# Kernel optimization log

Measured on AMD Instinct MI355X. Metric: run time of the kernel, lower is better.

## Reference

```python
import jax, jax.numpy as jnp
import numpy as np

EMBED = 192
EXPAND = 3
D1 = EMBED * EXPAND  # 576
RPE_IN = 32
LAYERS = 3
LAMBDA = 0.95


def _rpe_mlp(t, w0, b0, ws, bs, wo, bo):
    # t: (2n, 1) relative positions -> (2n, D1) Toeplitz coefficients
    h = t @ w0.T + b0
    for i in range(ws.shape[0]):
        h = jax.nn.relu(h) @ ws[i].T + bs[i]
    return jax.nn.relu(h) @ wo.T + bo


def _toeplitz(x, a):
    # Toeplitz matmul via length-2n circular convolution (FFT).
    # x: (B, n, d); a: (2n, d) coeffs ordered [t0, t1..t_{n-1}, pad, neg half]
    n = x.shape[1]
    m = 2 * n
    xf = jnp.fft.rfft(x, m, axis=1)
    af = jnp.fft.rfft(a, m, axis=0)
    return jnp.fft.irfft(xf * af[None], m, axis=1)[:, :n]


def _forward(x, p_w, p_b, q_w, q_b, v_w, v_b, o_w, o_b, slope,
             t1_w0, t1_b0, t1_ws, t1_bs, t1_wo, t1_bo,
             t2_w0, t2_b0, t2_ws, t2_bs, t2_wo, t2_bo):
    b, h, w, d = x.shape
    n = h  # square grid: h == w, rpe/decay built from n = x.shape[1]
    dt = x.dtype

    pos = jnp.arange(1, n, dtype=dt).reshape(-1, 1)          # (n-1, 1)
    zero = jnp.zeros((1, 1), dt)
    rpe_input = jnp.concatenate([zero, pos, zero, -pos], axis=0)  # (2n, 1)

    p = jax.nn.silu(x @ p_w.T + p_b)
    q = jax.nn.silu(x @ q_w.T + q_b)
    v = jax.nn.silu(x @ v_w.T + v_b)

    # decay mask: slope clamped to [0,1], blended with lambda, powered by |lag|
    sl = LAMBDA + (1.0 - LAMBDA) * jnp.clip(slope, 0.0, 1.0)  # (1, D1)
    idx = jnp.arange(1, n, dtype=dt).reshape(1, -1, 1)        # (1, n-1, 1)
    gamma = sl ** idx                                          # (1, n-1, D1)
    one = jnp.ones((1, 1, D1), dt)
    decay = jnp.concatenate([one, gamma, one, gamma[:, ::-1]], axis=1)[0]  # (2n, D1)

    a1 = _rpe_mlp(rpe_input, t1_w0, t1_b0, t1_ws, t1_bs, t1_wo, t1_bo) * decay
    a2 = _rpe_mlp(rpe_input, t2_w0, t2_b0, t2_ws, t2_bs, t2_wo, t2_bo) * decay

    qv = q * v                                                 # (b, h, w, D1)
    # axial mixing: tno1 along width, tno2 along height
    o1 = _toeplitz(qv.reshape(b * h, w, D1), a1).reshape(b, h, w, D1)
    o2 = _toeplitz(jnp.transpose(qv, (0, 2, 1, 3)).reshape(b * w, h, D1), a2)
    o2 = jnp.transpose(o2.reshape(b, w, h, D1), (0, 2, 1, 3))
    out = p * (o1 + o2)
    return out @ o_w.T + o_b


def setup_inputs() -> dict:
    key = jax.random.key(0)
    ks = jax.random.split(key, 8)

    def lin(k, out_d, in_d):
        k1, k2 = jax.random.split(k)
        s = 1.0 / np.sqrt(in_d)
        return (jax.random.uniform(k1, (out_d, in_d), jnp.float32, -s, s),
                jax.random.uniform(k2, (out_d,), jnp.float32, -s, s))

    x = jax.random.normal(ks[0], (8, 56, 56, EMBED), jnp.float32)
    p_w, p_b = lin(ks[1], D1, EMBED)
    q_w, q_b = lin(ks[2], D1, EMBED)
    v_w, v_b = lin(ks[3], D1, EMBED)
    o_w, o_b = lin(ks[4], EMBED, D1)
    # slope init: 1/arange(1, d1+1)^(1/(index+1)), index=0
    slope = (1.0 / jnp.arange(1, D1 + 1, dtype=jnp.float32)).reshape(1, -1)

    def tno_params(kb):
        kk = jax.random.split(kb, 2 + LAYERS)
        w0, b0 = lin(kk[0], RPE_IN, 1)
        ws, bs = [], []
        for i in range(LAYERS):
            wi, bi = lin(kk[1 + i], RPE_IN, RPE_IN)
            ws.append(wi); bs.append(bi)
        wo, bo = lin(kk[1 + LAYERS], D1, RPE_IN)
        return w0, b0, jnp.stack(ws), jnp.stack(bs), wo, bo

    t1 = tno_params(ks[5])
    t2 = tno_params(ks[6])
    return {"x": x, "p_w": p_w, "p_b": p_b, "q_w": q_w, "q_b": q_b,
            "v_w": v_w, "v_b": v_b, "o_w": o_w, "o_b": o_b, "slope": slope,
            "t1_w0": t1[0], "t1_b0": t1[1], "t1_ws": t1[2], "t1_bs": t1[3], "t1_wo": t1[4], "t1_bo": t1[5],
            "t2_w0": t2[0], "t2_b0": t2[1], "t2_ws": t2[2], "t2_bs": t2[3], "t2_wo": t2[4], "t2_bo": t2[5]}


def reference(x, p_w, p_b, q_w, q_b, v_w, v_b, o_w, o_b, slope,
              t1_w0, t1_b0, t1_ws, t1_bs, t1_wo, t1_bo,
              t2_w0, t2_b0, t2_ws, t2_bs, t2_wo, t2_bo):
    return _forward(x, p_w, p_b, q_w, q_b, v_w, v_b, o_w, o_b, slope,
                    t1_w0, t1_b0, t1_ws, t1_bs, t1_wo, t1_bo,
                    t2_w0, t2_b0, t2_ws, t2_bs, t2_wo, t2_bo)
```

## Files before the change

### kernel.cpp

```cpp
#include <hip/hip_runtime.h>
#include <hip/hip_bf16.h>
#include <math.h>

typedef unsigned short u16;
typedef short bf16x8 __attribute__((ext_vector_type(8)));
typedef float f32x4 __attribute__((ext_vector_type(4)));

#define NB 8
#define NN 56
#define M2 112
#define EMB 192
#define D1 576
#define TOK (NB*NN*NN)

__device__ __forceinline__ float bf2f(unsigned int u) {
    union { unsigned int i; float f; } v; v.i = u << 16; return v.f;
}
__device__ __forceinline__ u16 f2bf(float f) {
    union { float f; unsigned int i; } v; v.f = f;
    unsigned int x = v.i;
    return (u16)((x + 0x7fffu + ((x >> 16) & 1u)) >> 16);
}
__device__ __forceinline__ float silu(float x) {
    return x / (1.0f + __expf(-x));
}
__device__ __forceinline__ void async16(void* lds, const void* g) {
    __builtin_amdgcn_global_load_lds(
        (const __attribute__((address_space(1))) void*)g,
        (__attribute__((address_space(3))) void*)lds, 16, 0, 0);
}

#define XCH (TOK*EMB/4)
#define WCH (D1*EMB/4)
__global__ __launch_bounds__(256) void convert_kernel(
    const float* __restrict__ x,
    const float* __restrict__ pw, const float* __restrict__ qw,
    const float* __restrict__ vw, const float* __restrict__ ow,
    u16* __restrict__ xb, u16* __restrict__ wb, u16* __restrict__ owb)
{
    int tid = blockIdx.x * 256 + threadIdx.x;
    const float* src; u16* dst; int off;
    if (tid < XCH) { src = x; dst = xb; off = tid; }
    else {
        int r = tid - XCH;
        int seg = r / WCH; off = r % WCH;
        if (seg == 0)      { src = pw; dst = wb; }
        else if (seg == 1) { src = qw; dst = wb + D1*EMB; }
        else if (seg == 2) { src = vw; dst = wb + 2*D1*EMB; }
        else if (seg == 3) { src = ow; dst = owb; }
        else return;
    }
    float4 f = *(const float4*)(src + off * 4);
    ushort4 o;
    o.x = f2bf(f.x); o.y = f2bf(f.y); o.z = f2bf(f.z); o.w = f2bf(f.w);
    *(ushort4*)(dst + off * 4) = o;
}

__global__ __launch_bounds__(576) void rpe_kernel(
    const float* __restrict__ slope,
    const float* w0a, const float* b0a, const float* wsa, const float* bsa,
    const float* woa, const float* boa,
    const float* w0b, const float* b0b, const float* wsb, const float* bsb,
    const float* wob, const float* bob,
    float* __restrict__ A1, float* __restrict__ A2)
{
    int wq  = blockIdx.x / M2;
    int row = blockIdx.x % M2;
    const float* w0 = wq ? w0b : w0a;  const float* b0 = wq ? b0b : b0a;
    const float* ws = wq ? wsb : wsa;  const float* bs = wq ? bsb : bsa;
    const float* wo = wq ? wob : woa;  const float* bo = wq ? bob : boa;
    float* A = wq ? A2 : A1;

    float tval = (row == 0 || row == 56) ? 0.0f
               : (row < 56 ? (float)row : -(float)(row - 56));
    int kexp = (row == 0 || row == 56) ? 0 : (row < 56 ? row : 112 - row);

    __shared__ float h[32], g[32];
    int t = threadIdx.x;
    if (t < 32) h[t] = tval * w0[t] + b0[t];
    __syncthreads();
    for (int L = 0; L < 3; L++) {
        if (t < 32) g[t] = fmaxf(h[t], 0.0f);
        __syncthreads();
        float hn = 0.0f;
        if (t < 32) {
            hn = bs[L * 32 + t];
            for (int k = 0; k < 32; k++)
                hn = fmaf(g[k], ws[(L * 32 + t) * 32 + k], hn);
        }
        __syncthreads();
        if (t < 32) h[t] = hn;
        __syncthreads();
    }
    if (t < 32) g[t] = fmaxf(h[t], 0.0f);
    __syncthreads();

    float o = bo[t];
    for (int k = 0; k < 32; k++)
        o = fmaf(g[k], wo[t * 32 + k], o);

    float sl = slope[t];
    sl = 0.95f + 0.05f * fminf(fmaxf(sl, 0.0f), 1.0f);
    float dec = powf(sl, (float)kexp);
    A[row * D1 + t] = o * dec;
}

__global__ __launch_bounds__(256) void tbuild_kernel(
    const float* __restrict__ A1, const float* __restrict__ A2,
    u16* __restrict__ T1t, u16* __restrict__ T2t)
{
    int d = blockIdx.x;
    const float* src = blockIdx.y ? A2 : A1;
    u16* dst = blockIdx.y ? T2t : T1t;
    __shared__ float win[111];
    int t = threadIdx.x;
    if (t < 111) {
        int lag = t - 55;
        int rowi = lag + (lag < 0 ? 112 : 0);
        win[t] = src[rowi * D1 + d];
    }
    __syncthreads();
    int i = t >> 2, jq = (t & 3) * 16;
    u16 vals[16];
    #pragma unroll
    for (int jj = 0; jj < 16; jj++) {
        int j = jq + jj;
        float v = (i < 56 && j < 56) ? win[i - j + 55] : 0.0f;
        vals[jj] = f2bf(v);
    }
    u16* out = dst + ((size_t)d * 64 + i) * 64 + jq;
    *(uint4*)(out)     = *(uint4*)&vals[0];
    *(uint4*)(out + 8) = *(uint4*)&vals[8];
}

__global__ __launch_bounds__(256) void proj_kernel(
    const u16* __restrict__ xb, const u16* __restrict__ wb,
    const float* __restrict__ pb, const float* __restrict__ qb,
    const float* __restrict__ vb,
    u16* __restrict__ P_T, u16* __restrict__ QV_T)
{
    __shared__ u16 lds[20480];
    u16* As = lds;
    u16* Bs = lds + 8192;
    int m0 = blockIdx.x * 128, n0 = blockIdx.y * 64;
    int t = threadIdx.x;
    int l = t & 63, wave = t >> 6;
    int wm = wave >> 1, wn = wave & 1;
    int col16 = l & 15, q = l >> 4;

    f32x4 accp[4][2], accq[4][2], accv[4][2];
    #pragma unroll
    for (int i = 0; i < 4; i++)
        #pragma unroll
        for (int j = 0; j < 2; j++) {
            accp[i][j] = (f32x4){0,0,0,0};
            accq[i][j] = (f32x4){0,0,0,0};
            accv[i][j] = (f32x4){0,0,0,0};
        }

    for (int k0 = 0; k0 < EMB; k0 += 64) {
        #pragma unroll
        for (int ii = 0; ii < 4; ii++) {
            int slot = (ii * 4 + wave) * 64 + l;
            int r = slot >> 3, s = slot & 7;
            int g = s ^ (r & 7);
            async16(&As[slot * 8], xb + (m0 + r) * EMB + k0 + g * 8);
        }
        #pragma unroll
        for (int ii = 0; ii < 6; ii++) {
            int slot = (ii * 4 + wave) * 64 + l;
            int mat = slot >> 9, cc = slot & 511;
            int r = cc >> 3, s = cc & 7;
            int g = s ^ (r & 7);
            async16(&Bs[slot * 8],
                    wb + mat * (D1 * EMB) + (n0 + r) * EMB + k0 + g * 8);
        }
        __syncthreads();

        #pragma unroll
        for (int kk = 0; kk < 2; kk++) {
            bf16x8 af[4];
            #pragma unroll
            for (int mt = 0; mt < 4; mt++) {
                int row = wm * 64 + mt * 16 + col16;
                int sw = (q + 4 * kk) ^ (col16 & 7);
                af[mt] = *(const bf16x8*)&As[row * 64 + sw * 8];
            }
            bf16x8 bfr[3][2];
            #pragma unroll
            for (int mat = 0; mat < 3; mat++)
                #pragma unroll
                for (int nt = 0; nt < 2; nt++) {
                    int row = wn * 32 + nt * 16 + col16;
                    int sw = (q + 4 * kk) ^ (col16 & 7);
                    bfr[mat][nt] = *(const bf16x8*)&Bs[mat * 4096 + row * 64 + sw * 8];
                }
            #pragma unroll
            for (int mt = 0; mt < 4; mt++)
                #pragma unroll
                for (int nt = 0; nt < 2; nt++) {
                    accp[mt][nt] = __builtin_amdgcn_mfma_f32_16x16x32_bf16(
                        af[mt], bfr[0][nt], accp[mt][nt], 0, 0, 0);
                    accq[mt][nt] = __builtin_amdgcn_mfma_f32_16x16x32_bf16(
                        af[mt], bfr[1][nt], accq[mt][nt], 0, 0, 0);
                    accv[mt][nt] = __builtin_amdgcn_mfma_f32_16x16x32_bf16(
                        af[mt], bfr[2][nt], accv[mt][nt], 0, 0, 0);
                }
        }
        __syncthreads();
    }

    u16* scr = lds + wave * 2688;
    float pbv[2], qbv[2], vbv[2];
    #pragma unroll
    for (int nt = 0; nt < 2; nt++) {
        int n = n0 + wn * 32 + nt * 16 + col16;
        pbv[nt] = pb[n]; qbv[nt] = qb[n]; vbv[nt] = vb[n];
    }
    #pragma unroll
    for (int mt = 0; mt < 4; mt++)
        #pragma unroll
        for (int nt = 0; nt < 2; nt++)
            #pragma unroll
            for (int r = 0; r < 4; r++)
                scr[(mt * 16 + q * 4 + r) * 42 + nt * 16 + col16] =
                    f2bf(silu(accp[mt][nt][r] + pbv[nt]));
    #pragma unroll
    for (int dl = 0; dl < 32; dl++)
        P_T[(size_t)(n0 + wn * 32 + dl) * TOK + m0 + wm * 64 + l] =
            scr[l * 42 + dl];
    #pragma unroll
    for (int mt = 0; mt < 4; mt++)
        #pragma unroll
        for (int nt = 0; nt < 2; nt++)
            #pragma unroll
            for (int r = 0; r < 4; r++)
                scr[(mt * 16 + q * 4 + r) * 42 + nt * 16 + col16] =
                    f2bf(silu(accq[mt][nt][r] + qbv[nt]) *
                         silu(accv[mt][nt][r] + vbv[nt]));
    #pragma unroll
    for (int dl = 0; dl < 32; dl++)
        QV_T[(size_t)(n0 + wn * 32 + dl) * TOK + m0 + wm * 64 + l] =
            scr[l * 42 + dl];
}

__global__ __launch_bounds__(256) void tno_mfma(
    const u16* __restrict__ QV_T, const u16* __restrict__ T1t,
    const u16* __restrict__ T2t, const u16* __restrict__ P_T,
    u16* __restrict__ U_T)
{
    __shared__ u16 T1s[4096];
    __shared__ u16 T2s[4096];
    __shared__ u16 Qn[64 * 72];
    __shared__ u16 Qt[64 * 72];
    __shared__ float O1f[56 * 68];
    int d = blockIdx.x, b = blockIdx.y;
    int t = threadIdx.x;
    size_t base = (size_t)d * TOK + (size_t)b * 3136;

    #pragma unroll
    for (int k = 0; k < 2; k++) {
        int slot = t + k * 256;
        int i = slot >> 3, s = slot & 7;
        int g = s ^ (i & 7);
        async16(&T1s[slot * 8], T1t + ((size_t)d * 64 + i) * 64 + g * 8);
        async16(&T2s[slot * 8], T2t + ((size_t)d * 64 + i) * 64 + g * 8);
    }
    for (int c = t; c < 392; c += 256) {
        int h = c / 7, w8 = (c % 7) * 8;
        uint4 v = *(const uint4*)(QV_T + base + c * 8);
        *(uint4*)&Qn[h * 72 + w8] = v;
        u16 e[8];
        *(uint4*)e = v;
        #pragma unroll
        for (int k = 0; k < 8; k++)
            Qt[(w8 + k) * 72 + h] = e[k];
    }
    if (t < 56) {
        uint4 z = {0, 0, 0, 0};
        *(uint4*)&Qn[t * 72 + 56] = z;
        *(uint4*)&Qt[t * 72 + 56] = z;
    }
    __syncthreads();

    int l = t & 63, wave = t >> 6;
    int col16 = l & 15, q = l >> 4;

    f32x4 acc1[4], acc2[4];
    #pragma unroll
    for (int i = 0; i < 4; i++) { acc1[i] = (f32x4){0,0,0,0}; acc2[i] = (f32x4){0,0,0,0}; }

    #pragma unroll
    for (int kk = 0; kk < 2; kk++) {
        int sw = ((q + 4 * kk) ^ (col16 & 7)) * 8;
        bf16x8 bq1 = *(const bf16x8*)&Qn[(wave * 16 + col16) * 72 + kk * 32 + q * 8];
        bf16x8 bq2 = *(const bf16x8*)&Qt[(wave * 16 + col16) * 72 + kk * 32 + q * 8];
        #pragma unroll
        for (int mt = 0; mt < 4; mt++) {
            bf16x8 a1 = *(const bf16x8*)&T1s[(mt * 16 + col16) * 64 + sw];
            bf16x8 a2 = *(const bf16x8*)&T2s[(mt * 16 + col16) * 64 + sw];
            acc1[mt] = __builtin_amdgcn_mfma_f32_16x16x32_bf16(a1, bq1, acc1[mt], 0, 0, 0);
            acc2[mt] = __builtin_amdgcn_mfma_f32_16x16x32_bf16(a2, bq2, acc2[mt], 0, 0, 0);
        }
    }

    {
        int n = wave * 16 + col16;
        if (n < 56) {
            #pragma unroll
            for (int mt = 0; mt < 4; mt++)
                #pragma unroll
                for (int r = 0; r < 4; r++) {
                    int m = mt * 16 + q * 4 + r;
                    if (m < 56) O1f[n * 68 + m] = acc1[mt][r];
                }
        }
    }
    __syncthreads();
    {
        int n = wave * 16 + col16;
        if (n < 56) {
            #pragma unroll
            for (int mt = 0; mt < 4; mt++)
                #pragma unroll
                for (int r = 0; r < 4; r++) {
                    int m = mt * 16 + q * 4 + r;
                    if (m < 56) O1f[m * 68 + n] += acc2[mt][r];
                }
        }
    }
    __syncthreads();
    for (int c = t; c < 392; c += 256) {
        int h = c / 7, w8 = (c % 7) * 8;
        f32x4 s0 = *(const f32x4*)&O1f[h * 68 + w8];
        f32x4 s1 = *(const f32x4*)&O1f[h * 68 + w8 + 4];
        uint4 pv = *(const uint4*)(P_T + base + c * 8);
        u16 pe[8];
        *(uint4*)pe = pv;
        u16 ue[8];
        #pragma unroll
        for (int k = 0; k < 4; k++) ue[k] = f2bf(bf2f(pe[k]) * s0[k]);
        #pragma unroll
        for (int k = 0; k < 4; k++) ue[4 + k] = f2bf(bf2f(pe[4 + k]) * s1[k]);
        *(uint4*)(U_T + base + c * 8) = *(uint4*)ue;
    }
}

__global__ __launch_bounds__(256) void transp_kernel(
    const u16* __restrict__ U_T, u16* __restrict__ U)
{
    __shared__ u16 tile[64 * 72];
    int t = threadIdx.x;
    int t0 = blockIdx.x * 64;
    int d0 = blockIdx.y * 64;
    {
        int dr = t >> 2, c = t & 3;
        #pragma unroll
        for (int h = 0; h < 2; h++) {
            int cc = c + h * 4;
            uint4 v = *(const uint4*)(U_T + (size_t)(d0 + dr) * TOK + t0 + cc * 8);
            *(uint4*)&tile[dr * 72 + cc * 8] = v;
        }
    }
    __syncthreads();
    {
        int tr = t & 63, c4 = t >> 6;
        u16 vals[16];
        #pragma unroll
        for (int k = 0; k < 16; k++)
            vals[k] = tile[(c4 * 16 + k) * 72 + tr];
        u16* dst = U + (size_t)(t0 + tr) * D1 + d0 + c4 * 16;
        *(uint4*)(dst)     = *(uint4*)&vals[0];
        *(uint4*)(dst + 8) = *(uint4*)&vals[8];
    }
}

__global__ __launch_bounds__(256) void outproj_kernel(
    const u16* __restrict__ U, const u16* __restrict__ owb,
    const float* __restrict__ ob, float* __restrict__ out)
{
    __shared__ char ldsraw[36864];
    u16* As = (u16*)ldsraw;
    u16* Bs = (u16*)(ldsraw + 16384);
    int m0 = blockIdx.x * 128, n0 = blockIdx.y * 64;
    int t = threadIdx.x;
    int l = t & 63, wave = t >> 6;
    int wm = wave >> 1, wn = wave & 1;
    int col16 = l & 15, q = l >> 4;

    f32x4 acc[4][2];
    #pragma unroll
    for (int i = 0; i < 4; i++)
        #pragma unroll
        for (int j = 0; j < 2; j++) acc[i][j] = (f32x4){0,0,0,0};

    for (int k0 = 0; k0 < D1; k0 += 64) {
        #pragma unroll
        for (int ii = 0; ii < 4; ii++) {
            int slot = (ii * 4 + wave) * 64 + l;
            int r = slot >> 3, s = slot & 7;
            int g = s ^ (r & 7);
            async16(&As[slot * 8], U + (m0 + r) * D1 + k0 + g * 8);
        }
        #pragma unroll
        for (int ii = 0; ii < 2; ii++) {
            int slot = (ii * 4 + wave) * 64 + l;
            int r = slot >> 3, s = slot & 7;
            int g = s ^ (r & 7);
            async16(&Bs[slot * 8], owb + (n0 + r) * D1 + k0 + g * 8);
        }
        __syncthreads();

        #pragma unroll
        for (int kk = 0; kk < 2; kk++) {
            int sw = (q + 4 * kk) ^ (col16 & 7);
            bf16x8 af[4];
            #pragma unroll
            for (int mt = 0; mt < 4; mt++)
                af[mt] = *(const bf16x8*)&As[(wm * 64 + mt * 16 + col16) * 64 + sw * 8];
            bf16x8 bfr[2];
            #pragma unroll
            for (int nt = 0; nt < 2; nt++)
                bfr[nt] = *(const bf16x8*)&Bs[(wn * 32 + nt * 16 + col16) * 64 + sw * 8];
            #pragma unroll
            for (int mt = 0; mt < 4; mt++)
                #pragma unroll
                for (int nt = 0; nt < 2; nt++)
                    acc[mt][nt] = __builtin_amdgcn_mfma_f32_16x16x32_bf16(
                        af[mt], bfr[nt], acc[mt][nt], 0, 0, 0);
        }
        __syncthreads();
    }

    float* scr = (float*)ldsraw + wave * 2304;
    float obv[2];
    #pragma unroll
    for (int nt = 0; nt < 2; nt++)
        obv[nt] = ob[n0 + wn * 32 + nt * 16 + col16];
    #pragma unroll
    for (int mt = 0; mt < 4; mt++)
        #pragma unroll
        for (int nt = 0; nt < 2; nt++)
            #pragma unroll
            for (int r = 0; r < 4; r++)
                scr[(mt * 16 + q * 4 + r) * 36 + nt * 16 + col16] =
                    acc[mt][nt][r] + obv[nt];
    #pragma unroll
    for (int k = 0; k < 8; k++) {
        int row = k * 8 + (l >> 3), cs = (l & 7) * 4;
        f32x4 v = *(const f32x4*)&scr[row * 36 + cs];
        *(f32x4*)&out[(m0 + wm * 64 + row) * EMB + n0 + wn * 32 + cs] = v;
    }
}

extern "C" void kernel_launch(void* const* d_in, const int* in_sizes, int n_in,
                              void* d_out, int out_size, void* d_ws, size_t ws_size,
                              hipStream_t stream)
{
    (void)in_sizes; (void)n_in; (void)out_size; (void)ws_size;
    const float* x     = (const float*)d_in[0];
    const float* p_w   = (const float*)d_in[1];
    const float* p_b   = (const float*)d_in[2];
    const float* q_w   = (const float*)d_in[3];
    const float* q_b   = (const float*)d_in[4];
    const float* v_w   = (const float*)d_in[5];
    const float* v_b   = (const float*)d_in[6];
    const float* o_w   = (const float*)d_in[7];
    const float* o_b   = (const float*)d_in[8];
    const float* slope = (const float*)d_in[9];
    const float* t1_w0 = (const float*)d_in[10];
    const float* t1_b0 = (const float*)d_in[11];
    const float* t1_ws = (const float*)d_in[12];
    const float* t1_bs = (const float*)d_in[13];
    const float* t1_wo = (const float*)d_in[14];
    const float* t1_bo = (const float*)d_in[15];
    const float* t2_w0 = (const float*)d_in[16];
    const float* t2_b0 = (const float*)d_in[17];
    const float* t2_ws = (const float*)d_in[18];
    const float* t2_bs = (const float*)d_in[19];
    const float* t2_wo = (const float*)d_in[20];
    const float* t2_bo = (const float*)d_in[21];

    char* ws = (char*)d_ws;
    float* A1  = (float*)ws;
    float* A2  = (float*)(ws + 258048);
    u16*   PU  = (u16*)(ws + 516096);
    u16*   QVT = (u16*)(ws + 29417472);
    u16*   UT  = (u16*)(ws + 58318848);
    u16*   xb  = (u16*)(ws + 87220224);
    u16*   wb  = (u16*)(ws + 96854016);
    u16*   owb = (u16*)(ws + 97517568);
    u16*   T1t = (u16*)(ws + 97738752);
    u16*   T2t = (u16*)(ws + 102457344);

    convert_kernel<<<(XCH + 4*WCH + 255) / 256, 256, 0, stream>>>(
        x, p_w, q_w, v_w, o_w, xb, wb, owb);
    rpe_kernel<<<224, 576, 0, stream>>>(slope,
        t1_w0, t1_b0, t1_ws, t1_bs, t1_wo, t1_bo,
        t2_w0, t2_b0, t2_ws, t2_bs, t2_wo, t2_bo, A1, A2);
    tbuild_kernel<<<dim3(576, 2), 256, 0, stream>>>(A1, A2, T1t, T2t);
    proj_kernel<<<dim3(TOK / 128, D1 / 64), 256, 0, stream>>>(
        xb, wb, p_b, q_b, v_b, PU, QVT);
    tno_mfma<<<dim3(D1, NB), 256, 0, stream>>>(QVT, T1t, T2t, PU, UT);
    transp_kernel<<<dim3(TOK / 64, D1 / 64), 256, 0, stream>>>(UT, PU);
    outproj_kernel<<<dim3(TOK / 128, EMB / 64), 256, 0, stream>>>(
        PU, owb, o_b, (float*)d_out);
}
```

Baseline: 218.1 us.

## Fuse x bf16 conversion into projection loads and batch two images per TNO block

The separate pass that converts x to bf16 is dropped. The projection kernel now loads fp32 x directly, converts it in registers and stores it swizzled into LDS, which saves a full write and re-read of the bf16 copy of x. In exchange, x is reloaded in fp32 by each of the 9 column-tile blocks, and those loads are synchronous rather than async. Separately, each tno_mfma block now handles two batch images, so the Toeplitz tiles loaded into LDS are reused and the grid is halved, at the cost of less parallelism.

Result: slower. 228.4 us (+4.7%).

```diff
diff --git a/kernel.cpp b/kernel.cpp
--- a/kernel.cpp
+++ b/kernel.cpp
@@ -30,26 +30,20 @@
         (__attribute__((address_space(3))) void*)lds, 16, 0, 0);
 }
 
-#define XCH (TOK*EMB/4)
 #define WCH (D1*EMB/4)
-__global__ __launch_bounds__(256) void convert_kernel(
-    const float* __restrict__ x,
+__global__ __launch_bounds__(256) void convertw_kernel(
     const float* __restrict__ pw, const float* __restrict__ qw,
     const float* __restrict__ vw, const float* __restrict__ ow,
-    u16* __restrict__ xb, u16* __restrict__ wb, u16* __restrict__ owb)
+    u16* __restrict__ wb, u16* __restrict__ owb)
 {
     int tid = blockIdx.x * 256 + threadIdx.x;
-    const float* src; u16* dst; int off;
-    if (tid < XCH) { src = x; dst = xb; off = tid; }
-    else {
-        int r = tid - XCH;
-        int seg = r / WCH; off = r % WCH;
-        if (seg == 0)      { src = pw; dst = wb; }
-        else if (seg == 1) { src = qw; dst = wb + D1*EMB; }
-        else if (seg == 2) { src = vw; dst = wb + 2*D1*EMB; }
-        else if (seg == 3) { src = ow; dst = owb; }
-        else return;
-    }
+    int seg = tid / WCH, off = tid % WCH;
+    const float* src; u16* dst;
+    if (seg == 0)      { src = pw; dst = wb; }
+    else if (seg == 1) { src = qw; dst = wb + D1*EMB; }
+    else if (seg == 2) { src = vw; dst = wb + 2*D1*EMB; }
+    else if (seg == 3) { src = ow; dst = owb; }
+    else return;
     float4 f = *(const float4*)(src + off * 4);
     ushort4 o;
     o.x = f2bf(f.x); o.y = f2bf(f.y); o.z = f2bf(f.z); o.w = f2bf(f.w);
@@ -134,7 +128,7 @@
 }
 
 __global__ __launch_bounds__(256) void proj_kernel(
-    const u16* __restrict__ xb, const u16* __restrict__ wb,
+    const float* __restrict__ x, const u16* __restrict__ wb,
     const float* __restrict__ pb, const float* __restrict__ qb,
     const float* __restrict__ vb,
     u16* __restrict__ P_T, u16* __restrict__ QV_T)
@@ -160,13 +154,6 @@
 
     for (int k0 = 0; k0 < EMB; k0 += 64) {
         #pragma unroll
-        for (int ii = 0; ii < 4; ii++) {
-            int slot = (ii * 4 + wave) * 64 + l;
-            int r = slot >> 3, s = slot & 7;
-            int g = s ^ (r & 7);
-            async16(&As[slot * 8], xb + (m0 + r) * EMB + k0 + g * 8);
-        }
-        #pragma unroll
         for (int ii = 0; ii < 6; ii++) {
             int slot = (ii * 4 + wave) * 64 + l;
             int mat = slot >> 9, cc = slot & 511;
@@ -174,6 +161,18 @@
             int g = s ^ (r & 7);
             async16(&Bs[slot * 8],
                     wb + mat * (D1 * EMB) + (n0 + r) * EMB + k0 + g * 8);
+        }
+        #pragma unroll
+        for (int ii = 0; ii < 4; ii++) {
+            int c = t + ii * 256;
+            int r = c >> 3, s = c & 7;
+            int g = s ^ (r & 7);
+            const float* src = x + (m0 + r) * EMB + k0 + g * 8;
+            float4 f0 = *(const float4*)src;
+            float4 f1 = *(const float4*)(src + 4);
+            u16 e[8] = { f2bf(f0.x), f2bf(f0.y), f2bf(f0.z), f2bf(f0.w),
+                         f2bf(f1.x), f2bf(f1.y), f2bf(f1.z), f2bf(f1.w) };
+            *(uint4*)&As[c * 8] = *(uint4*)e;
         }
         __syncthreads();
 
@@ -254,9 +253,10 @@
     __shared__ u16 Qn[64 * 72];
     __shared__ u16 Qt[64 * 72];
     __shared__ float O1f[56 * 68];
-    int d = blockIdx.x, b = blockIdx.y;
+    int d = blockIdx.x;
     int t = threadIdx.x;
-    size_t base = (size_t)d * TOK + (size_t)b * 3136;
+    int l = t & 63, wave = t >> 6;
+    int col16 = l & 15, q = l >> 4;
 
     #pragma unroll
     for (int k = 0; k < 2; k++) {
@@ -266,83 +266,87 @@
         async16(&T1s[slot * 8], T1t + ((size_t)d * 64 + i) * 64 + g * 8);
         async16(&T2s[slot * 8], T2t + ((size_t)d * 64 + i) * 64 + g * 8);
     }
-    for (int c = t; c < 392; c += 256) {
-        int h = c / 7, w8 = (c % 7) * 8;
-        uint4 v = *(const uint4*)(QV_T + base + c * 8);
-        *(uint4*)&Qn[h * 72 + w8] = v;
-        u16 e[8];
-        *(uint4*)e = v;
-        #pragma unroll
-        for (int k = 0; k < 8; k++)
-            Qt[(w8 + k) * 72 + h] = e[k];
-    }
-    if (t < 56) {
-        uint4 z = {0, 0, 0, 0};
-        *(uint4*)&Qn[t * 72 + 56] = z;
-        *(uint4*)&Qt[t * 72 + 56] = z;
-    }
-    __syncthreads();
-
-    int l = t & 63, wave = t >> 6;
-    int col16 = l & 15, q = l >> 4;
-
-    f32x4 acc1[4], acc2[4];
-    #pragma unroll
-    for (int i = 0; i < 4; i++) { acc1[i] = (f32x4){0,0,0,0}; acc2[i] = (f32x4){0,0,0,0}; }
-
-    #pragma unroll
-    for (int kk = 0; kk < 2; kk++) {
-        int sw = ((q + 4 * kk) ^ (col16 & 7)) * 8;
-        bf16x8 bq1 = *(const bf16x8*)&Qn[(wave * 16 + col16) * 72 + kk * 32 + q * 8];
-        bf16x8 bq2 = *(const bf16x8*)&Qt[(wave * 16 + col16) * 72 + kk * 32 + q * 8];
-        #pragma unroll
-        for (int mt = 0; mt < 4; mt++) {
-            bf16x8 a1 = *(const bf16x8*)&T1s[(mt * 16 + col16) * 64 + sw];
-            bf16x8 a2 = *(const bf16x8*)&T2s[(mt * 16 + col16) * 64 + sw];
-            acc1[mt] = __builtin_amdgcn_mfma_f32_16x16x32_bf16(a1, bq1, acc1[mt], 0, 0, 0);
-            acc2[mt] = __builtin_amdgcn_mfma_f32_16x16x32_bf16(a2, bq2, acc2[mt], 0, 0, 0);
-        }
-    }
-
-    {
-        int n = wave * 16 + col16;
-        if (n < 56) {
-            #pragma unroll
-            for (int mt = 0; mt < 4; mt++)
+
+    for (int bi = 0; bi < 2; bi++) {
+        int b = blockIdx.y * 2 + bi;
+        size_t base = (size_t)d * TOK + (size_t)b * 3136;
+        __syncthreads();
+
+        for (int c = t; c < 392; c += 256) {
+            int h = c / 7, w8 = (c % 7) * 8;
+            uint4 v = *(const uint4*)(QV_T + base + c * 8);
+            *(uint4*)&Qn[h * 72 + w8] = v;
+            u16 e[8];
+            *(uint4*)e = v;
+            #pragma unroll
+            for (int k = 0; k < 8; k++)
+                Qt[(w8 + k) * 72 + h] = e[k];
+        }
+        if (t < 56) {
+            uint4 z = {0, 0, 0, 0};
+            *(uint4*)&Qn[t * 72 + 56] = z;
+            *(uint4*)&Qt[t * 72 + 56] = z;
+        }
+        __syncthreads();
+
+        f32x4 acc1[4], acc2[4];
+        #pragma unroll
+        for (int i = 0; i < 4; i++) { acc1[i] = (f32x4){0,0,0,0}; acc2[i] = (f32x4){0,0,0,0}; }
+
+        #pragma unroll
+        for (int kk = 0; kk < 2; kk++) {
+            int sw = ((q + 4 * kk) ^ (col16 & 7)) * 8;
+            bf16x8 bq1 = *(const bf16x8*)&Qn[(wave * 16 + col16) * 72 + kk * 32 + q * 8];
+            bf16x8 bq2 = *(const bf16x8*)&Qt[(wave * 16 + col16) * 72 + kk * 32 + q * 8];
+            #pragma unroll
+            for (int mt = 0; mt < 4; mt++) {
+                bf16x8 a1 = *(const bf16x8*)&T1s[(mt * 16 + col16) * 64 + sw];
+                bf16x8 a2 = *(const bf16x8*)&T2s[(mt * 16 + col16) * 64 + sw];
+                acc1[mt] = __builtin_amdgcn_mfma_f32_16x16x32_bf16(a1, bq1, acc1[mt], 0, 0, 0);
+                acc2[mt] = __builtin_amdgcn_mfma_f32_16x16x32_bf16(a2, bq2, acc2[mt], 0, 0, 0);
+            }
+        }
+
+        {
+            int n = wave * 16 + col16;
+            if (n < 56) {
                 #pragma unroll
-                for (int r = 0; r < 4; r++) {
-                    int m = mt * 16 + q * 4 + r;
-                    if (m < 56) O1f[n * 68 + m] = acc1[mt][r];
-                }
-        }
-    }
-    __syncthreads();
-    {
-        int n = wave * 16 + col16;
-        if (n < 56) {
-            #pragma unroll
-            for (int mt = 0; mt < 4; mt++)
+                for (int mt = 0; mt < 4; mt++)
+                    #pragma unroll
+                    for (int r = 0; r < 4; r++) {
+                        int m = mt * 16 + q * 4 + r;
+                        if (m < 56) O1f[n * 68 + m] = acc1[mt][r];
+                    }
+            }
+        }
+        __syncthreads();
+        {
+            int n = wave * 16 + col16;
+            if (n < 56) {
                 #pragma unroll
-                for (int r = 0; r < 4; r++) {
-                    int m = mt * 16 + q * 4 + r;
-                    if (m < 56) O1f[m * 68 + n] += acc2[mt][r];
-                }
-        }
-    }
-    __syncthreads();
-    for (int c = t; c < 392; c += 256) {
-        int h = c / 7, w8 = (c % 7) * 8;
-        f32x4 s0 = *(const f32x4*)&O1f[h * 68 + w8];
-        f32x4 s1 = *(const f32x4*)&O1f[h * 68 + w8 + 4];
-        uint4 pv = *(const uint4*)(P_T + base + c * 8);
-        u16 pe[8];
-        *(uint4*)pe = pv;
-        u16 ue[8];
-        #pragma unroll
-        for (int k = 0; k < 4; k++) ue[k] = f2bf(bf2f(pe[k]) * s0[k]);
-        #pragma unroll
-        for (int k = 0; k < 4; k++) ue[4 + k] = f2bf(bf2f(pe[4 + k]) * s1[k]);
-        *(uint4*)(U_T + base + c * 8) = *(uint4*)ue;
+                for (int mt = 0; mt < 4; mt++)
+                    #pragma unroll
+                    for (int r = 0; r < 4; r++) {
+                        int m = mt * 16 + q * 4 + r;
+                        if (m < 56) O1f[m * 68 + n] += acc2[mt][r];
+                    }
+            }
+        }
+        __syncthreads();
+        for (int c = t; c < 392; c += 256) {
+            int h = c / 7, w8 = (c % 7) * 8;
+            f32x4 s0 = *(const f32x4*)&O1f[h * 68 + w8];
+            f32x4 s1 = *(const f32x4*)&O1f[h * 68 + w8 + 4];
+            uint4 pv = *(const uint4*)(P_T + base + c * 8);
+            u16 pe[8];
+            *(uint4*)pe = pv;
+            u16 ue[8];
+            #pragma unroll
+            for (int k = 0; k < 4; k++) ue[k] = f2bf(bf2f(pe[k]) * s0[k]);
+            #pragma unroll
+            for (int k = 0; k < 4; k++) ue[4 + k] = f2bf(bf2f(pe[4 + k]) * s1[k]);
+            *(uint4*)(U_T + base + c * 8) = *(uint4*)ue;
+        }
     }
 }
 
@@ -487,21 +491,20 @@
     u16*   PU  = (u16*)(ws + 516096);
     u16*   QVT = (u16*)(ws + 29417472);
     u16*   UT  = (u16*)(ws + 58318848);
-    u16*   xb  = (u16*)(ws + 87220224);
     u16*   wb  = (u16*)(ws + 96854016);
     u16*   owb = (u16*)(ws + 97517568);
     u16*   T1t = (u16*)(ws + 97738752);
     u16*   T2t = (u16*)(ws + 102457344);
 
-    convert_kernel<<<(XCH + 4*WCH + 255) / 256, 256, 0, stream>>>(
-        x, p_w, q_w, v_w, o_w, xb, wb, owb);
+    convertw_kernel<<<(4 * WCH + 255) / 256, 256, 0, stream>>>(
+        p_w, q_w, v_w, o_w, wb, owb);
     rpe_kernel<<<224, 576, 0, stream>>>(slope,
         t1_w0, t1_b0, t1_ws, t1_bs, t1_wo, t1_bo,
         t2_w0, t2_b0, t2_ws, t2_bs, t2_wo, t2_bo, A1, A2);
     tbuild_kernel<<<dim3(576, 2), 256, 0, stream>>>(A1, A2, T1t, T2t);
     proj_kernel<<<dim3(TOK / 128, D1 / 64), 256, 0, stream>>>(
-        xb, wb, p_b, q_b, v_b, PU, QVT);
-    tno_mfma<<<dim3(D1, NB), 256, 0, stream>>>(QVT, T1t, T2t, PU, UT);
+        x, wb, p_b, q_b, v_b, PU, QVT);
+    tno_mfma<<<dim3(D1, NB / 2), 256, 0, stream>>>(QVT, T1t, T2t, PU, UT);
     transp_kernel<<<dim3(TOK / 64, D1 / 64), 256, 0, stream>>>(UT, PU);
     outproj_kernel<<<dim3(TOK / 128, EMB / 64), 256, 0, stream>>>(
         PU, owb, o_b, (float*)d_out);
```
